# Kernel tuning notes

Hardware: AMD Instinct MI355X
Metric: run time of the kernel (lower is better)

Reference implementation:

```python
import jax, jax.numpy as jnp
import numpy as np
import math

EMB_DIM = 3        # positional embedding dim of the implicit Hyena filter
FILTER_ORDER = 64  # hidden width of the implicit filter MLP


def rmsnorm(x, w, eps=1e-8):
    return x * jax.lax.rsqrt(jnp.mean(x * x, axis=-1, keepdims=True) + eps) * w


def _implicit_filter(L, D, mlp_w1, mlp_b1, freq1, mlp_w2, mlp_b2, freq2, mlp_w3):
    # positional embedding (emb_dim=3): [t, Re exp(-i f w), Im exp(-i f w)], bands=1
    t = jnp.linspace(0.0, 1.0, L)[:, None]                               # (L,1)
    w = 2.0 * math.pi * jnp.linspace(0.0, L - 1.0, L)[:, None] / L       # (L,1)
    f = jnp.linspace(1e-4, 0.0, 1)[None, :]                              # (1,1)
    ang = f * w
    z = jnp.concatenate([t, jnp.cos(ang), -jnp.sin(ang)], axis=-1)       # (L,3)
    # implicit filter MLP with Sin activations
    h = jnp.sin(freq1 * (z @ mlp_w1.T + mlp_b1))
    h = jnp.sin(freq2 * (h @ mlp_w2.T + mlp_b2))
    h = h @ mlp_w3.T                                                     # (L,D)
    # exponential modulation (modulate=True)
    fast, slow, target = 0.3, 1.5, 1e-2
    max_decay = math.log(target) / fast
    min_decay = math.log(target) / slow
    deltas = jnp.linspace(min_decay, max_decay, D)[None, :]              # (1,D)
    h = h * jnp.exp(-t * jnp.abs(deltas))
    return h.T                                                           # (D,L)


def _fftconv(v, k, bias):
    # causal long conv via zero-padded FFT. v: (B,D,L), k: (D,L), bias: (D,)
    L = v.shape[-1]
    n = 2 * L
    kf = jnp.fft.rfft(k, n=n) / n
    y = jnp.fft.irfft(jnp.fft.rfft(v, n=n) * kf, n=n, norm="forward")[..., :L]
    return y + v * bias[None, :, None]


def _block(x, norm_in_w, in_proj_w, in_proj_b, short_filter_w, short_filter_b,
           mlp_w1, mlp_b1, freq1, mlp_w2, mlp_b2, freq2, mlp_w3, filter_bias,
           out_proj_w, out_proj_b, norm_w, ffn_w1, ffn_b1, ffn_w2, ffn_b2):
    B, L, D = x.shape
    xn = rmsnorm(x, norm_in_w)
    # Hyena operator
    u = (xn @ in_proj_w.T + in_proj_b).transpose(0, 2, 1)                # (B,3D,L)
    uc = jax.lax.conv_general_dilated(
        u, short_filter_w, (1,), [(2, 0)],
        feature_group_count=3 * D, dimension_numbers=("NCH", "OIH", "NCH"))
    uc = uc + short_filter_b[None, :, None]                              # causal k=3 depthwise
    x0, x1, v = jnp.split(uc, 3, axis=1)                                 # (B,D,L) each
    k = _implicit_filter(L, D, mlp_w1, mlp_b1, freq1, mlp_w2, mlp_b2, freq2, mlp_w3)
    v = _fftconv(v * x1, k, filter_bias)                                 # gate, long conv
    y = (v * x0).transpose(0, 2, 1) @ out_proj_w.T + out_proj_b          # gate, out proj
    # residual + FFN
    h = y + x
    o = rmsnorm(h, norm_w)
    o = jax.nn.gelu(o @ ffn_w1.T + ffn_b1) @ ffn_w2.T + ffn_b2
    return o + h


def setup_inputs():
    key = jax.random.key(0)
    B, L, D = 4, 2048, 1024
    ks = jax.random.split(key, 12)

    def lin(k, out_d, in_d):
        return jax.random.normal(k, (out_d, in_d), jnp.float32) * (1.0 / math.sqrt(in_d))

    return {
        "x": jax.random.normal(ks[0], (B, L, D), jnp.float32),
        "norm_in_w": jnp.ones((D,), jnp.float32),
        "in_proj_w": lin(ks[1], 3 * D, D),
        "in_proj_b": jnp.zeros((3 * D,), jnp.float32),
        "short_filter_w": jax.random.normal(ks[2], (3 * D, 1, 3), jnp.float32) / math.sqrt(3.0),
        "short_filter_b": jnp.zeros((3 * D,), jnp.float32),
        "mlp_w1": lin(ks[3], FILTER_ORDER, EMB_DIM),
        "mlp_b1": jnp.zeros((FILTER_ORDER,), jnp.float32),
        "freq1": jnp.ones((FILTER_ORDER,), jnp.float32),
        "mlp_w2": lin(ks[4], FILTER_ORDER, FILTER_ORDER),
        "mlp_b2": jnp.zeros((FILTER_ORDER,), jnp.float32),
        "freq2": jnp.ones((FILTER_ORDER,), jnp.float32),
        "mlp_w3": lin(ks[5], D, FILTER_ORDER),
        "filter_bias": jax.random.normal(ks[6], (D,), jnp.float32),
        "out_proj_w": lin(ks[7], D, D),
        "out_proj_b": jnp.zeros((D,), jnp.float32),
        "norm_w": jnp.ones((D,), jnp.float32),
        "ffn_w1": lin(ks[8], 2 * D, D),
        "ffn_b1": jnp.zeros((2 * D,), jnp.float32),
        "ffn_w2": lin(ks[9], D, 2 * D),
        "ffn_b2": jnp.zeros((D,), jnp.float32),
    }


def reference(x, norm_in_w, in_proj_w, in_proj_b, short_filter_w, short_filter_b,
              mlp_w1, mlp_b1, freq1, mlp_w2, mlp_b2, freq2, mlp_w3, filter_bias,
              out_proj_w, out_proj_b, norm_w, ffn_w1, ffn_b1, ffn_w2, ffn_b2):
    return _block(x, norm_in_w, in_proj_w, in_proj_b, short_filter_w, short_filter_b,
                  mlp_w1, mlp_b1, freq1, mlp_w2, mlp_b2, freq2, mlp_w3, filter_bias,
                  out_proj_w, out_proj_b, norm_w, ffn_w1, ffn_b1, ffn_w2, ffn_b2)
```

## Files before the change

kernel.cpp:

```cpp
#include <hip/hip_runtime.h>
#include <hip/hip_bf16.h>
#include <cstddef>

#define BB 4
#define LL 2048
#define DD 1024
#define MM (BB*LL)
#define KF_STRIDE 2056

#define SWZ(a) ((a) ^ (((a) >> 4) & 12))

typedef __bf16 bf16_t;
typedef __attribute__((ext_vector_type(8))) __bf16 bf16x8;
typedef __attribute__((ext_vector_type(4))) __bf16 bf16x4;
typedef __attribute__((ext_vector_type(4))) float f32x4;

#define GLD_LDS16(gp, lp) __builtin_amdgcn_global_load_lds(                 \
    (const __attribute__((address_space(1))) unsigned int*)(gp),            \
    (__attribute__((address_space(3))) unsigned int*)(lp), 16, 0, 0)

__device__ __forceinline__ float gelu_tanh(float x) {
    const float c = 0.7978845608028654f;
    float t = tanhf(c * (x + 0.044715f * x * x * x));
    return 0.5f * x * (1.0f + t);
}

__device__ __forceinline__ float2 cmul(float2 a, float2 b) {
    return make_float2(a.x * b.x - a.y * b.y, a.x * b.y + a.y * b.x);
}
__device__ __forceinline__ float2 cadd(float2 a, float2 b) {
    return make_float2(a.x + b.x, a.y + b.y);
}
__device__ __forceinline__ float2 csub(float2 a, float2 b) {
    return make_float2(a.x - b.x, a.y - b.y);
}
__device__ __forceinline__ float2 cmuli(float2 z, float s) {
    return make_float2(-s * z.y, s * z.x);
}

__global__ __launch_bounds__(256) void cast_all_kernel(
    const float* __restrict__ s0, const float* __restrict__ s1,
    const float* __restrict__ s2, const float* __restrict__ s3,
    bf16_t* __restrict__ d0, bf16_t* __restrict__ d1,
    bf16_t* __restrict__ d2, bf16_t* __restrict__ d3)
{
    const int b = blockIdx.x;
    const float* s; bf16_t* d; int base;
    if (b < 3072)      { s = s0; d = d0; base = b; }
    else if (b < 4096) { s = s1; d = d1; base = b - 3072; }
    else if (b < 6144) { s = s2; d = d2; base = b - 4096; }
    else               { s = s3; d = d3; base = b - 6144; }
    const int i = (base * 256 + threadIdx.x) * 4;
    const float4 v = *(const float4*)(s + i);
    bf16x4 o;
    o[0] = (bf16_t)v.x; o[1] = (bf16_t)v.y; o[2] = (bf16_t)v.z; o[3] = (bf16_t)v.w;
    *(bf16x4*)(d + i) = o;
}

__global__ __launch_bounds__(256) void rmsnorm_bf16_kernel(
    const float* __restrict__ in, const float* __restrict__ w,
    bf16_t* __restrict__ out)
{
    const int row = blockIdx.x;
    const float4* ip = (const float4*)(in + (size_t)row * DD);
    float4 v = ip[threadIdx.x];
    float ss = v.x*v.x + v.y*v.y + v.z*v.z + v.w*v.w;
    #pragma unroll
    for (int off = 32; off > 0; off >>= 1) ss += __shfl_down(ss, off, 64);
    __shared__ float sums[4];
    const int wid = threadIdx.x >> 6;
    if ((threadIdx.x & 63) == 0) sums[wid] = ss;
    __syncthreads();
    const float tot = sums[0] + sums[1] + sums[2] + sums[3];
    const float scale = rsqrtf(tot * (1.0f / (float)DD) + 1e-8f);
    const float4 wv = ((const float4*)w)[threadIdx.x];
    bf16x4 o;
    o[0] = (bf16_t)(v.x * scale * wv.x);
    o[1] = (bf16_t)(v.y * scale * wv.y);
    o[2] = (bf16_t)(v.z * scale * wv.z);
    o[3] = (bf16_t)(v.w * scale * wv.w);
    *(bf16x4*)(out + (size_t)row * DD + threadIdx.x * 4) = o;
}

template<int EPI, bool BF16OUT, bool BIASROW = false>
__global__ __launch_bounds__(256) void gemm_mfma_kernel(
    const bf16_t* __restrict__ A,
    const bf16_t* __restrict__ W,
    const float* __restrict__ bias,
    const float* __restrict__ res,
    float* __restrict__ Cf,
    bf16_t* __restrict__ Cb,
    int M, int N, int K)
{
    __shared__ __align__(16) bf16_t As[128 * 32];
    __shared__ __align__(16) bf16_t Ws[128 * 32];
    const int tid  = threadIdx.x;
    const int bm   = blockIdx.y * 128;
    const int bn   = blockIdx.x * 128;
    const int lane = tid & 63;
    const int wave = tid >> 6;
    const int wr   = (wave >> 1) * 64;
    const int wc   = (wave & 1) * 64;

    const int lrow = tid >> 2;
    const int lcol = (tid & 3) * 8;

    const bf16_t* Ag = A + (size_t)(bm + lrow) * K + lcol;
    const bf16_t* Wg = W + (size_t)(bn + lrow) * K + lcol;
    bf16_t* AsL0 = As + lrow * 32 + lcol;
    bf16_t* AsL1 = As + (64 + lrow) * 32 + lcol;
    bf16_t* WsL0 = Ws + lrow * 32 + lcol;
    bf16_t* WsL1 = Ws + (64 + lrow) * 32 + lcol;

    f32x4 acc[4][4] = {};

    const int fr = lane & 15;
    const int fc = (lane >> 4) * 8;

    for (int k0 = 0; k0 < K; k0 += 32) {
        GLD_LDS16(Ag + k0,                AsL0);
        GLD_LDS16(Ag + (size_t)64*K + k0, AsL1);
        GLD_LDS16(Wg + k0,                WsL0);
        GLD_LDS16(Wg + (size_t)64*K + k0, WsL1);
        __syncthreads();

        bf16x8 af[4], wf[4];
        #pragma unroll
        for (int i = 0; i < 4; ++i)
            af[i] = *(const bf16x8*)(As + (wr + i*16 + fr) * 32 + fc);
        #pragma unroll
        for (int j = 0; j < 4; ++j)
            wf[j] = *(const bf16x8*)(Ws + (wc + j*16 + fr) * 32 + fc);
        #pragma unroll
        for (int i = 0; i < 4; ++i)
            #pragma unroll
            for (int j = 0; j < 4; ++j)
                acc[i][j] = __builtin_amdgcn_mfma_f32_16x16x32_bf16(
                    af[i], wf[j], acc[i][j], 0, 0, 0);
        __syncthreads();
    }

    const int fq = lane >> 4;
    #pragma unroll
    for (int i = 0; i < 4; ++i) {
        const int row0 = bm + wr + i*16 + fq*4;
        #pragma unroll
        for (int j = 0; j < 4; ++j) {
            const int col = bn + wc + j*16 + fr;
            const float bcol = BIASROW ? 0.0f : bias[col];
            #pragma unroll
            for (int r = 0; r < 4; ++r) {
                float v = acc[i][j][r] + (BIASROW ? bias[row0 + r] : bcol);
                if constexpr (EPI == 2) v = gelu_tanh(v);
                if constexpr (EPI == 1) v += res[(size_t)(row0 + r) * N + col];
                if constexpr (BF16OUT)
                    Cb[(size_t)(row0 + r) * N + col] = (bf16_t)v;
                else
                    Cf[(size_t)(row0 + r) * N + col] = v;
            }
        }
    }
}

__global__ __launch_bounds__(256) void shortfilter_kernel(
    const bf16_t* __restrict__ ut, const float* __restrict__ sw,
    const float* __restrict__ sb, bf16_t* __restrict__ x0t,
    float* __restrict__ vin)
{
    const int d = blockIdx.x;
    const int c0 = d, c1 = DD + d, c2 = 2 * DD + d;
    const float w0a = sw[c0*3+0], w0b = sw[c0*3+1], w0c = sw[c0*3+2], b0 = sb[c0];
    const float w1a = sw[c1*3+0], w1b = sw[c1*3+1], w1c = sw[c1*3+2], b1 = sb[c1];
    const float w2a = sw[c2*3+0], w2b = sw[c2*3+1], w2c = sw[c2*3+2], b2 = sb[c2];
    const bf16_t* r0 = ut + (size_t)c0 * MM;
    const bf16_t* r1 = ut + (size_t)c1 * MM;
    const bf16_t* r2 = ut + (size_t)c2 * MM;
    bf16_t* o0 = x0t + (size_t)d * MM;
    float*  o1 = vin + (size_t)d * MM;
    for (int m = threadIdx.x; m < MM; m += 256) {
        const int l = m & (LL - 1);
        float v0 = w0c * (float)r0[m] + b0;
        float v1 = w1c * (float)r1[m] + b1;
        float v2 = w2c * (float)r2[m] + b2;
        if (l >= 1) {
            v0 += w0b * (float)r0[m-1];
            v1 += w1b * (float)r1[m-1];
            v2 += w2b * (float)r2[m-1];
        }
        if (l >= 2) {
            v0 += w0a * (float)r0[m-2];
            v1 += w1a * (float)r1[m-2];
            v2 += w2a * (float)r2[m-2];
        }
        o0[m] = (bf16_t)v0;
        o1[m] = v2 * v1;
    }
}

__global__ __launch_bounds__(256) void filtermlp_kernel(
    const float* __restrict__ w1, const float* __restrict__ b1,
    const float* __restrict__ f1, const float* __restrict__ w2,
    const float* __restrict__ b2, const float* __restrict__ f2,
    float* __restrict__ h2t)
{
    __shared__ float w2s[64 * 64];
    for (int i = threadIdx.x; i < 64 * 64; i += 256) w2s[i] = w2[i];
    __syncthreads();
    const int l = blockIdx.x * 256 + threadIdx.x;
    const float t = (float)l / (float)(LL - 1);
    const float ang = 1e-4f * 6.283185307179586f * (float)l / (float)LL;
    const float z0 = t, z1 = cosf(ang), z2 = -sinf(ang);
    float h1[64];
    #pragma unroll
    for (int j = 0; j < 64; ++j) {
        const float s = w1[j*3+0]*z0 + w1[j*3+1]*z1 + w1[j*3+2]*z2 + b1[j];
        h1[j] = sinf(f1[j] * s);
    }
    for (int j = 0; j < 64; ++j) {
        float s = b2[j];
        #pragma unroll
        for (int jj = 0; jj < 64; ++jj) s += w2s[j*64 + jj] * h1[jj];
        h2t[j * LL + l] = sinf(f2[j] * s);
    }
}

__global__ __launch_bounds__(256) void filtermod_kernel(
    const float* __restrict__ w3, const float* __restrict__ h2t,
    float* __restrict__ kfilt)
{
    __shared__ float w3s[32 * 64];
    const int d0 = blockIdx.y * 32;
    const int l  = blockIdx.x * 256 + threadIdx.x;
    for (int i = threadIdx.x; i < 32 * 64; i += 256) w3s[i] = w3[d0 * 64 + i];
    __syncthreads();
    float acc[32] = {};
    for (int j = 0; j < 64; ++j) {
        const float v = h2t[j * LL + l];
        #pragma unroll
        for (int dd = 0; dd < 32; ++dd) acc[dd] += w3s[dd*64 + j] * v;
    }
    const float t = (float)l / (float)(LL - 1);
    const float min_decay = -3.0701134573253944f;
    const float max_decay = -15.350567286626972f;
    #pragma unroll
    for (int dd = 0; dd < 32; ++dd) {
        const int d = d0 + dd;
        const float delta = fabsf(min_decay + (max_decay - min_decay) * (float)d / (float)(DD - 1));
        kfilt[(size_t)d * LL + l] = acc[dd] * expf(-t * delta);
    }
}

template<int SIGN>
__device__ __forceinline__ void fft4096_r8_ip(float2* __restrict__ buf)
{
    const float fs = (float)SIGN;
    const float RH = 0.7071067811865476f;
    const int tid = threadIdx.x;
    #pragma unroll
    for (int t = 0; t < 4; ++t) {
        const int ls = 3 * t;
        const int s  = 1 << ls;
        const float theta = fs * 6.283185307179586f / (float)(4096 >> ls);
        float2 a[8];
        #pragma unroll
        for (int m = 0; m < 8; ++m) a[m] = buf[SWZ(tid + m * 512)];
        __syncthreads();
        const int p = tid >> ls;
        const int q = tid & (s - 1);
        float sn, cs;
        __sincosf(theta * (float)p, &sn, &cs);
        const float2 W1 = make_float2(cs, sn);
        const float2 W2 = cmul(W1, W1);
        const float2 W3 = cmul(W2, W1);
        const float2 W4 = cmul(W2, W2);
        const float2 W5 = cmul(W4, W1);
        const float2 W6 = cmul(W4, W2);
        const float2 W7 = cmul(W4, W3);
        const float2 es = cadd(a[0], a[4]), ed = csub(a[0], a[4]);
        const float2 fs2 = cadd(a[2], a[6]), fd = csub(a[2], a[6]);
        const float2 E0 = cadd(es, fs2);
        const float2 E1 = cadd(ed, cmuli(fd, fs));
        const float2 E2 = csub(es, fs2);
        const float2 E3 = csub(ed, cmuli(fd, fs));
        const float2 os = cadd(a[1], a[5]), od = csub(a[1], a[5]);
        const float2 gs = cadd(a[3], a[7]), gd = csub(a[3], a[7]);
        const float2 O0 = cadd(os, gs);
        const float2 O1 = cadd(od, cmuli(gd, fs));
        const float2 O2 = csub(os, gs);
        const float2 O3 = csub(od, cmuli(gd, fs));
        const float2 T0 = O0;
        const float2 T1 = make_float2(RH * (O1.x - fs * O1.y), RH * (fs * O1.x + O1.y));
        const float2 T2 = cmuli(O2, fs);
        const float2 T3 = make_float2(RH * (-O3.x - fs * O3.y), RH * (fs * O3.x - O3.y));
        const int o = q + (p << (ls + 3));
        buf[SWZ(o)]         = cadd(E0, T0);
        buf[SWZ(o + s)]     = cmul(W1, cadd(E1, T1));
        buf[SWZ(o + 2*s)]   = cmul(W2, cadd(E2, T2));
        buf[SWZ(o + 3*s)]   = cmul(W3, cadd(E3, T3));
        buf[SWZ(o + 4*s)]   = cmul(W4, csub(E0, T0));
        buf[SWZ(o + 5*s)]   = cmul(W5, csub(E1, T1));
        buf[SWZ(o + 6*s)]   = cmul(W6, csub(E2, T2));
        buf[SWZ(o + 7*s)]   = cmul(W7, csub(E3, T3));
        __syncthreads();
    }
}

__global__ __launch_bounds__(512, 4) void kfft_kernel(
    const float* __restrict__ kfilt, float2* __restrict__ Kf)
{
    __shared__ float2 fb[4096];
    const int d0 = blockIdx.x * 2;
    const float* k0 = kfilt + (size_t)d0 * LL;
    const float* k1 = k0 + LL;
    const float inv = 1.0f / 4096.0f;
    const int tid = threadIdx.x;
    for (int i = tid; i < 2048; i += 512) {
        fb[SWZ(i)]        = make_float2(k0[i] * inv, k1[i] * inv);
        fb[SWZ(i + 2048)] = make_float2(0.f, 0.f);
    }
    __syncthreads();
    fft4096_r8_ip<-1>(fb);
    float2* o0 = Kf + (size_t)d0 * KF_STRIDE;
    float2* o1 = o0 + KF_STRIDE;
    for (int k = tid; k <= 2048; k += 512) {
        const float2 z1 = fb[SWZ(k)];
        const float2 z2 = fb[SWZ((4096 - k) & 4095)];
        o0[k] = make_float2(0.5f * (z1.x + z2.x), 0.5f * (z1.y - z2.y));
        o1[k] = make_float2(0.5f * (z1.y + z2.y), 0.5f * (z2.x - z1.x));
    }
}

__global__ __launch_bounds__(512, 4) void fftconv_kernel(
    float* __restrict__ vio, const float2* __restrict__ Kf,
    const float* __restrict__ fbias)
{
    __shared__ float2 fb[4096];
    const int blk = blockIdx.x;
    const int d   = blk >> 1;
    float* v1 = vio + (size_t)(2 * blk) * LL;
    float* v2 = v1 + LL;
    const int tid = threadIdx.x;
    for (int i = tid; i < 2048; i += 512) {
        fb[SWZ(i)]        = make_float2(v1[i], v2[i]);
        fb[SWZ(i + 2048)] = make_float2(0.f, 0.f);
    }
    __syncthreads();
    fft4096_r8_ip<-1>(fb);
    const float2* kf = Kf + (size_t)d * KF_STRIDE;
    for (int i = tid; i < 4096; i += 512) {
        float2 k;
        if (i <= 2048) k = kf[i];
        else { const float2 t = kf[4096 - i]; k = make_float2(t.x, -t.y); }
        fb[SWZ(i)] = cmul(fb[SWZ(i)], k);
    }
    __syncthreads();
    fft4096_r8_ip<1>(fb);
    const float bias = fbias[d];
    for (int i = tid; i < 2048; i += 512) {
        const float2 zy = fb[SWZ(i)];
        v1[i] = zy.x + bias * v1[i];
        v2[i] = zy.y + bias * v2[i];
    }
}

__global__ __launch_bounds__(256) void gate_transpose_kernel(
    const float* __restrict__ y, const bf16_t* __restrict__ x0t,
    bf16_t* __restrict__ g)
{
    __shared__ float tile[32][33];
    const int b  = blockIdx.z;
    const int l0 = blockIdx.x * 32;
    const int d0 = blockIdx.y * 32;
    const int tx  = threadIdx.x & 31;
    const int tyb = threadIdx.x >> 5;
    #pragma unroll
    for (int i = 0; i < 4; ++i) {
        const int dy = tyb + i * 8;
        const size_t src = ((size_t)(d0 + dy) * BB + b) * LL + l0 + tx;
        tile[dy][tx] = y[src] * (float)x0t[src];
    }
    __syncthreads();
    #pragma unroll
    for (int i = 0; i < 4; ++i) {
        const int ly = tyb + i * 8;
        g[((size_t)(b * LL + l0 + ly)) * DD + d0 + tx] = (bf16_t)tile[tx][ly];
    }
}

extern "C" void kernel_launch(void* const* d_in, const int* in_sizes, int n_in,
                              void* d_out, int out_size, void* d_ws, size_t ws_size,
                              hipStream_t stream)
{
    (void)in_sizes; (void)n_in; (void)out_size; (void)ws_size;
    const float* x   = (const float*)d_in[0];
    const float* nw0 = (const float*)d_in[1];
    const float* ipw = (const float*)d_in[2];
    const float* ipb = (const float*)d_in[3];
    const float* sfw = (const float*)d_in[4];
    const float* sfb = (const float*)d_in[5];
    const float* w1  = (const float*)d_in[6];
    const float* b1  = (const float*)d_in[7];
    const float* f1  = (const float*)d_in[8];
    const float* w2  = (const float*)d_in[9];
    const float* b2  = (const float*)d_in[10];
    const float* f2  = (const float*)d_in[11];
    const float* w3  = (const float*)d_in[12];
    const float* fbv = (const float*)d_in[13];
    const float* opw = (const float*)d_in[14];
    const float* opb = (const float*)d_in[15];
    const float* nw1 = (const float*)d_in[16];
    const float* fw1 = (const float*)d_in[17];
    const float* fb1 = (const float*)d_in[18];
    const float* fw2 = (const float*)d_in[19];
    const float* fb2 = (const float*)d_in[20];
    float* out = (float*)d_out;

    float* ws = (float*)d_ws;
    bf16_t* utb    = (bf16_t*)ws;
    bf16_t* gatedb = (bf16_t*)ws;
    float*  h      = ws + 4194304;
    bf16_t* midb   = (bf16_t*)(ws + 12582912);
    bf16_t* xnb    = (bf16_t*)(ws + 25165824);
    bf16_t* x0tb   = (bf16_t*)(ws + 29360128);
    float*  vio    = ws + 37748736;
    float*  kfilt  = ws + 46137344;
    float2* Kf     = (float2*)(ws + 48234496);
    bf16_t* ipwb   = (bf16_t*)(ws + 52445184);
    bf16_t* opwb   = ipwb + 3145728;
    bf16_t* fw1b   = opwb + 1048576;
    bf16_t* fw2b   = fw1b + 2097152;
    float*  h2t    = ws + 56639488;

    cast_all_kernel<<<8192, 256, 0, stream>>>(ipw, opw, fw1, fw2,
                                              ipwb, opwb, fw1b, fw2b);
    filtermlp_kernel<<<LL/256, 256, 0, stream>>>(w1, b1, f1, w2, b2, f2, h2t);
    filtermod_kernel<<<dim3(LL/256, DD/32), 256, 0, stream>>>(w3, h2t, kfilt);
    kfft_kernel<<<DD/2, 512, 0, stream>>>(kfilt, Kf);
    rmsnorm_bf16_kernel<<<MM, 256, 0, stream>>>(x, nw0, xnb);
    gemm_mfma_kernel<0, true, true><<<dim3(MM/128, 3072/128), 256, 0, stream>>>(
        ipwb, xnb, ipb, nullptr, nullptr, utb, 3*DD, MM, DD);
    shortfilter_kernel<<<DD, 256, 0, stream>>>(utb, sfw, sfb, x0tb, vio);
    fftconv_kernel<<<BB*DD/2, 512, 0, stream>>>(vio, Kf, fbv);
    gate_transpose_kernel<<<dim3(LL/32, DD/32, BB), 256, 0, stream>>>(vio, x0tb, gatedb);
    gemm_mfma_kernel<1, false><<<dim3(DD/128, MM/128), 256, 0, stream>>>(
        gatedb, opwb, opb, x, h, nullptr, MM, DD, DD);
    rmsnorm_bf16_kernel<<<MM, 256, 0, stream>>>(h, nw1, xnb);
    gemm_mfma_kernel<2, true><<<dim3(2*DD/128, MM/128), 256, 0, stream>>>(
        xnb, fw1b, fb1, nullptr, nullptr, midb, MM, 2*DD, DD);
    gemm_mfma_kernel<1, false><<<dim3(DD/128, MM/128), 256, 0, stream>>>(
        midb, fw2b, fb2, h, out, nullptr, MM, DD, 2*DD);
}
```

Baseline: 581.0 us.

## Double GEMM K-tile to 64 and XOR-swizzle LDS layout for conflict-free reads

The MFMA GEMM kernel now stages a 64-wide K slice per iteration instead of 32, which halves the number of barrier pairs and loop iterations. The LDS tile is laid out with an XOR swizzle on 16-byte groups, so the fragment reads from shared memory avoid bank conflicts. The global-to-LDS load addressing is rewritten to write the swizzled layout directly. In exchange, LDS use per block doubles, which may reduce occupancy, and there is still no double buffering.

Result: faster. 544.0 us (-6.4%).

```diff
diff --git a/kernel.cpp b/kernel.cpp
--- a/kernel.cpp
+++ b/kernel.cpp
@@ -92,8 +92,8 @@
     bf16_t* __restrict__ Cb,
     int M, int N, int K)
 {
-    __shared__ __align__(16) bf16_t As[128 * 32];
-    __shared__ __align__(16) bf16_t Ws[128 * 32];
+    __shared__ __align__(16) bf16_t As[128 * 64];
+    __shared__ __align__(16) bf16_t Ws[128 * 64];
     const int tid  = threadIdx.x;
     const int bm   = blockIdx.y * 128;
     const int bn   = blockIdx.x * 128;
@@ -102,41 +102,50 @@
     const int wr   = (wave >> 1) * 64;
     const int wc   = (wave & 1) * 64;
 
-    const int lrow = tid >> 2;
-    const int lcol = (tid & 3) * 8;
-
-    const bf16_t* Ag = A + (size_t)(bm + lrow) * K + lcol;
-    const bf16_t* Wg = W + (size_t)(bn + lrow) * K + lcol;
-    bf16_t* AsL0 = As + lrow * 32 + lcol;
-    bf16_t* AsL1 = As + (64 + lrow) * 32 + lcol;
-    bf16_t* WsL0 = Ws + lrow * 32 + lcol;
-    bf16_t* WsL1 = Ws + (64 + lrow) * 32 + lcol;
+    int srow[4], sqg[4];
+    #pragma unroll
+    for (int c = 0; c < 4; ++c) {
+        const int p = c * 256 + tid;
+        srow[c] = p >> 3;
+        sqg[c]  = (((p & 7) ^ (srow[c] & 7)) << 3);
+    }
 
     f32x4 acc[4][4] = {};
 
     const int fr = lane & 15;
     const int fc = (lane >> 4) * 8;
 
-    for (int k0 = 0; k0 < K; k0 += 32) {
-        GLD_LDS16(Ag + k0,                AsL0);
-        GLD_LDS16(Ag + (size_t)64*K + k0, AsL1);
-        GLD_LDS16(Wg + k0,                WsL0);
-        GLD_LDS16(Wg + (size_t)64*K + k0, WsL1);
+    for (int k0 = 0; k0 < K; k0 += 64) {
+        #pragma unroll
+        for (int c = 0; c < 4; ++c) {
+            GLD_LDS16(A + (size_t)(bm + srow[c]) * K + k0 + sqg[c],
+                      As + c * 2048 + tid * 8);
+            GLD_LDS16(W + (size_t)(bn + srow[c]) * K + k0 + sqg[c],
+                      Ws + c * 2048 + tid * 8);
+        }
         __syncthreads();
 
-        bf16x8 af[4], wf[4];
-        #pragma unroll
-        for (int i = 0; i < 4; ++i)
-            af[i] = *(const bf16x8*)(As + (wr + i*16 + fr) * 32 + fc);
-        #pragma unroll
-        for (int j = 0; j < 4; ++j)
-            wf[j] = *(const bf16x8*)(Ws + (wc + j*16 + fr) * 32 + fc);
-        #pragma unroll
-        for (int i = 0; i < 4; ++i)
+        #pragma unroll
+        for (int ks = 0; ks < 64; ks += 32) {
+            const int q = (ks + fc) >> 3;
+            bf16x8 af[4], wf[4];
             #pragma unroll
-            for (int j = 0; j < 4; ++j)
-                acc[i][j] = __builtin_amdgcn_mfma_f32_16x16x32_bf16(
-                    af[i], wf[j], acc[i][j], 0, 0, 0);
+            for (int i = 0; i < 4; ++i) {
+                const int r = wr + i*16 + fr;
+                af[i] = *(const bf16x8*)(As + r * 64 + ((q ^ (r & 7)) << 3));
+            }
+            #pragma unroll
+            for (int j = 0; j < 4; ++j) {
+                const int r = wc + j*16 + fr;
+                wf[j] = *(const bf16x8*)(Ws + r * 64 + ((q ^ (r & 7)) << 3));
+            }
+            #pragma unroll
+            for (int i = 0; i < 4; ++i)
+                #pragma unroll
+                for (int j = 0; j < 4; ++j)
+                    acc[i][j] = __builtin_amdgcn_mfma_f32_16x16x32_bf16(
+                        af[i], wf[j], acc[i][j], 0, 0, 0);
+        }
         __syncthreads();
     }
 
```
